# Kernel tuning notes

Measured on AMD Instinct MI355X. Metric: run time of the kernel, lower is better.

The kernel has to match this reference:

```python
import jax, jax.numpy as jnp
import numpy as np

EPS = 1e-8

def setup_inputs() -> dict:
    key = jax.random.key(0)
    k1, k2 = jax.random.split(key)
    x1 = jax.random.normal(k1, (16, 4096, 256), dtype=jnp.float32)
    x2 = jax.random.normal(k2, (16, 4096, 256), dtype=jnp.float32)
    return {"x1": x1, "x2": x2}

def _l2_normalize(x):
    # matches F.normalize / torch norm-with-clamp: x / max(||x||, eps)
    n = jnp.linalg.norm(x, axis=-1, keepdims=True)
    return x / jnp.maximum(n, EPS)

def reference(x1, x2):
    # cosine distance: mean over all segment pairs of (1 - cos_sim)
    # mean_{i,j} (1 - x1n_i . x2n_j) == 1 - (mean_i x1n_i) . (mean_j x2n_j)
    # -- algebraically identical to the original per-batch mm + mean,
    # but avoids materializing the O(n_seg^2) similarity matrix.
    n_batch, embedding_dim = x1.shape[0], x1.shape[-1]
    x1 = x1.reshape(n_batch, -1, embedding_dim)
    x2 = x2.reshape(n_batch, -1, embedding_dim)
    x1n = _l2_normalize(x1)  # (B, S, D)
    x2n = _l2_normalize(x2)
    m1 = x1n.mean(axis=1)    # (B, D)
    m2 = x2n.mean(axis=1)    # (B, D)
    return 1.0 - jnp.einsum('bd,bd->b', m1, m2)  # (B,)
```

## Files before the change

kernel.cpp:

```cpp
#include <hip/hip_runtime.h>


constexpr int D = 256;
constexpr int S = 4096;
constexpr int B = 16;
constexpr int BLOCKS_PER_SEQ = 64;
constexpr int WAVES_PER_BLOCK = 4;
constexpr int WAVES_PER_SEQ  = BLOCKS_PER_SEQ * WAVES_PER_BLOCK;
constexpr int PAIRS_PER_WAVE = (S / 2) / WAVES_PER_SEQ;
constexpr int NSEQ  = 2 * B;
constexpr int NBLK1 = NSEQ * BLOCKS_PER_SEQ;
constexpr float EPS2 = 1e-16f;

template <int CTRL>
__device__ __forceinline__ float dpp_add(float x) {
    int xi = __builtin_bit_cast(int, x);
    int yi = __builtin_amdgcn_update_dpp(0, xi, CTRL, 0xf, 0xf, true);
    return x + __builtin_bit_cast(float, yi);
}

__device__ __forceinline__ float half_reduce(float x) {
    x = dpp_add<0xB1>(x);
    x = dpp_add<0x4E>(x);
    x = dpp_add<0x141>(x);
    x = dpp_add<0x140>(x);
    int xi = __builtin_bit_cast(int, x);
    int yi = __builtin_amdgcn_ds_swizzle(xi, 0x401F);
    return x + __builtin_bit_cast(float, yi);
}

template <bool USE_PARTIALS>
__global__ __launch_bounds__(256) void row_norm_sum_kernel(
    const float* __restrict__ x1, const float* __restrict__ x2,
    float* __restrict__ sums )
{
    const int seq  = blockIdx.x / BLOCKS_PER_SEQ;
    const int blk  = blockIdx.x % BLOCKS_PER_SEQ;
    const int w    = threadIdx.x >> 6;
    const int lane = threadIdx.x & 63;
    const int half = lane >> 5;
    const int l    = lane & 31;
    const int wv   = blk * WAVES_PER_BLOCK + w;

    const int batch = seq >> 1;
    const float* __restrict__ src = (seq & 1) ? x2 : x1;
    const float* base = src + (size_t)batch * S * D
                            + (size_t)(2 * wv + half) * D + 4 * l;

    float4 vlo[PAIRS_PER_WAVE], vhi[PAIRS_PER_WAVE];
    #pragma unroll
    for (int p = 0; p < PAIRS_PER_WAVE; ++p) {
        const float* a = base + (size_t)p * (WAVES_PER_SEQ * 2 * D);
        vlo[p] = *(const float4*)a;
        vhi[p] = *(const float4*)(a + 128);
    }

    float4 acc_lo = make_float4(0.f, 0.f, 0.f, 0.f);
    float4 acc_hi = make_float4(0.f, 0.f, 0.f, 0.f);
    #pragma unroll
    for (int p = 0; p < PAIRS_PER_WAVE; ++p) {
        float ss = vlo[p].x * vlo[p].x + vlo[p].y * vlo[p].y
                 + vlo[p].z * vlo[p].z + vlo[p].w * vlo[p].w
                 + vhi[p].x * vhi[p].x + vhi[p].y * vhi[p].y
                 + vhi[p].z * vhi[p].z + vhi[p].w * vhi[p].w;
        ss = half_reduce(ss);
        const float s = rsqrtf(fmaxf(ss, EPS2));
        acc_lo.x += vlo[p].x * s;  acc_lo.y += vlo[p].y * s;
        acc_lo.z += vlo[p].z * s;  acc_lo.w += vlo[p].w * s;
        acc_hi.x += vhi[p].x * s;  acc_hi.y += vhi[p].y * s;
        acc_hi.z += vhi[p].z * s;  acc_hi.w += vhi[p].w * s;
    }

    __shared__ float red[WAVES_PER_BLOCK][2][D];
    *(float4*)&red[w][half][4 * l]       = acc_lo;
    *(float4*)&red[w][half][128 + 4 * l] = acc_hi;
    __syncthreads();

    const int t = threadIdx.x;
    float val = 0.f;
    #pragma unroll
    for (int ww = 0; ww < WAVES_PER_BLOCK; ++ww)
        val += red[ww][0][t] + red[ww][1][t];
    if (USE_PARTIALS) {
        sums[(size_t)blockIdx.x * D + t] = val;
    } else {
        atomicAdd(&sums[(size_t)seq * D + t], val);
    }
}

__global__ __launch_bounds__(256) void finalize_partials_kernel(
    const float* __restrict__ partials, float* __restrict__ out)
{
    const int b = blockIdx.x;
    const int t = threadIdx.x;
    const int w = t >> 6, lane = t & 63;

    const float* p1 = partials + ((size_t)(2 * b + 0) * BLOCKS_PER_SEQ) * D + t;
    const float* p2 = partials + ((size_t)(2 * b + 1) * BLOCKS_PER_SEQ) * D + t;
    float s1 = 0.f, s2 = 0.f;
    #pragma unroll 8
    for (int k = 0; k < BLOCKS_PER_SEQ; ++k) {
        s1 += p1[(size_t)k * D];
        s2 += p2[(size_t)k * D];
    }
    float d = s1 * s2;
    #pragma unroll
    for (int m = 1; m < 64; m <<= 1) d += __shfl_xor(d, m, 64);

    __shared__ float r[WAVES_PER_BLOCK];
    if (lane == 0) r[w] = d;
    __syncthreads();
    if (t == 0) {
        const float inv = 1.0f / ((float)S * (float)S);
        out[b] = 1.0f - (r[0] + r[1] + r[2] + r[3]) * inv;
    }
}

__global__ __launch_bounds__(64) void finalize_kernel(
    const float* __restrict__ sums, float* __restrict__ out)
{
    const int b = blockIdx.x;
    const int lane = threadIdx.x;
    const float4 a = *(const float4*)(sums + (size_t)(2 * b + 0) * D + lane * 4);
    const float4 c = *(const float4*)(sums + (size_t)(2 * b + 1) * D + lane * 4);
    float d = a.x * c.x + a.y * c.y + a.z * c.z + a.w * c.w;
    #pragma unroll
    for (int m = 1; m < 64; m <<= 1) d += __shfl_xor(d, m, 64);
    if (lane == 0) {
        const float inv = 1.0f / ((float)S * (float)S);
        out[b] = 1.0f - d * inv;
    }
}

extern "C" void kernel_launch(void* const* d_in, const int* in_sizes, int n_in,
                              void* d_out, int out_size, void* d_ws, size_t ws_size,
                              hipStream_t stream) {
    const float* x1 = (const float*)d_in[0];
    const float* x2 = (const float*)d_in[1];
    float* out = (float*)d_out;
    float* ws = (float*)d_ws;

    const size_t partial_bytes = (size_t)NBLK1 * D * sizeof(float);
    if (ws_size >= partial_bytes) {
        row_norm_sum_kernel<true><<<NBLK1, 256, 0, stream>>>(x1, x2, ws);
        finalize_partials_kernel<<<B, 256, 0, stream>>>(ws, out);
    } else {
        hipMemsetAsync(ws, 0, (size_t)NSEQ * D * sizeof(float), stream);
        row_norm_sum_kernel<false><<<NBLK1, 256, 0, stream>>>(x1, x2, ws);
        finalize_kernel<<<B, 64, 0, stream>>>(ws, out);
    }
}
```

Measured before the change: 147.8 us.

## Stream rows through an LDS ring with async global-to-LDS loads

The row-norm kernel now runs one wave per block (2048 blocks of 64 threads), each handling 64 contiguous rows. Rows are loaded with global_load_lds into a four-slot LDS ring, two slots ahead, with explicit vmcnt waits. Before, each wave held 16 rows in registers, all loaded up front. The cross-wave LDS reduction and barrier are replaced by a single cross-half shuffle. The aim is to overlap loads with compute and cut register pressure, at the cost of far fewer resident waves and fewer bytes in flight per CU.

```diff
diff --git a/kernel.cpp b/kernel.cpp
--- a/kernel.cpp
+++ b/kernel.cpp
@@ -4,13 +4,23 @@
 constexpr int D = 256;
 constexpr int S = 4096;
 constexpr int B = 16;
-constexpr int BLOCKS_PER_SEQ = 64;
-constexpr int WAVES_PER_BLOCK = 4;
-constexpr int WAVES_PER_SEQ  = BLOCKS_PER_SEQ * WAVES_PER_BLOCK;
-constexpr int PAIRS_PER_WAVE = (S / 2) / WAVES_PER_SEQ;
-constexpr int NSEQ  = 2 * B;
-constexpr int NBLK1 = NSEQ * BLOCKS_PER_SEQ;
+constexpr int NSEQ = 2 * B;
+constexpr int NROWS = NSEQ * S;
+
+constexpr int NBLK = 2048;
+constexpr int BLOCKS_PER_SEQ = NBLK / NSEQ;
+constexpr int ROWS_PER_BLOCK = NROWS / NBLK;
+constexpr int ROWS_PER_SLOT = 4;
+constexpr int SLOT_BYTES = ROWS_PER_SLOT * D * 4;
+constexpr int NSLOTS = 4;
+constexpr int NITER = ROWS_PER_BLOCK / ROWS_PER_SLOT;
 constexpr float EPS2 = 1e-16f;
+
+__device__ __forceinline__ void dma_row(const float* g, char* lds) {
+    __builtin_amdgcn_global_load_lds(
+        (const __attribute__((address_space(1))) void*)g,
+        (__attribute__((address_space(3))) void*)lds, 16, 0, 0);
+}
 
 template <int CTRL>
 __device__ __forceinline__ float dpp_add(float x) {
@@ -30,61 +40,90 @@
 }
 
 template <bool USE_PARTIALS>
-__global__ __launch_bounds__(256) void row_norm_sum_kernel(
+__global__ __launch_bounds__(64) void row_norm_sum_kernel(
     const float* __restrict__ x1, const float* __restrict__ x2,
     float* __restrict__ sums )
 {
-    const int seq  = blockIdx.x / BLOCKS_PER_SEQ;
-    const int blk  = blockIdx.x % BLOCKS_PER_SEQ;
-    const int w    = threadIdx.x >> 6;
-    const int lane = threadIdx.x & 63;
+    __shared__ char ring[NSLOTS * SLOT_BYTES];
+
+    const int lane = threadIdx.x;
     const int half = lane >> 5;
     const int l    = lane & 31;
-    const int wv   = blk * WAVES_PER_BLOCK + w;
 
-    const int batch = seq >> 1;
-    const float* __restrict__ src = (seq & 1) ? x2 : x1;
-    const float* base = src + (size_t)batch * S * D
-                            + (size_t)(2 * wv + half) * D + 4 * l;
+    const int seq = blockIdx.x / BLOCKS_PER_SEQ;
+    const int r0  = (blockIdx.x % BLOCKS_PER_SEQ) * ROWS_PER_BLOCK;
+    const float* __restrict__ src =
+        ((seq & 1) ? x2 : x1) + (size_t)(seq >> 1) * S * D + (size_t)r0 * D;
+    const float* gl = src + 4 * lane;
 
-    float4 vlo[PAIRS_PER_WAVE], vhi[PAIRS_PER_WAVE];
     #pragma unroll
-    for (int p = 0; p < PAIRS_PER_WAVE; ++p) {
-        const float* a = base + (size_t)p * (WAVES_PER_SEQ * 2 * D);
-        vlo[p] = *(const float4*)a;
-        vhi[p] = *(const float4*)(a + 128);
-    }
+    for (int s = 0; s < 2; ++s)
+        #pragma unroll
+        for (int r = 0; r < ROWS_PER_SLOT; ++r)
+            dma_row(gl + (size_t)(s * ROWS_PER_SLOT + r) * D,
+                    ring + s * SLOT_BYTES + r * 1024);
 
     float4 acc_lo = make_float4(0.f, 0.f, 0.f, 0.f);
     float4 acc_hi = make_float4(0.f, 0.f, 0.f, 0.f);
+
     #pragma unroll
-    for (int p = 0; p < PAIRS_PER_WAVE; ++p) {
-        float ss = vlo[p].x * vlo[p].x + vlo[p].y * vlo[p].y
-                 + vlo[p].z * vlo[p].z + vlo[p].w * vlo[p].w
-                 + vhi[p].x * vhi[p].x + vhi[p].y * vhi[p].y
-                 + vhi[p].z * vhi[p].z + vhi[p].w * vhi[p].w;
-        ss = half_reduce(ss);
-        const float s = rsqrtf(fmaxf(ss, EPS2));
-        acc_lo.x += vlo[p].x * s;  acc_lo.y += vlo[p].y * s;
-        acc_lo.z += vlo[p].z * s;  acc_lo.w += vlo[p].w * s;
-        acc_hi.x += vhi[p].x * s;  acc_hi.y += vhi[p].y * s;
-        acc_hi.z += vhi[p].z * s;  acc_hi.w += vhi[p].w * s;
+    for (int i = 0; i < NITER; ++i) {
+        if (i < NITER - 1) asm volatile("s_waitcnt vmcnt(4)" ::: "memory");
+        else               asm volatile("s_waitcnt vmcnt(0)" ::: "memory");
+
+        if (i + 2 < NITER) {
+            char* sl = ring + ((i + 2) & (NSLOTS - 1)) * SLOT_BYTES;
+            #pragma unroll
+            for (int r = 0; r < ROWS_PER_SLOT; ++r)
+                dma_row(gl + (size_t)((i + 2) * ROWS_PER_SLOT + r) * D,
+                        sl + r * 1024);
+        }
+
+        const char* sl = ring + (i & (NSLOTS - 1)) * SLOT_BYTES;
+        #pragma unroll
+        for (int p = 0; p < 2; ++p) {
+            const float* rowp = (const float*)(sl + p * 2048 + half * 1024);
+            const float4 vlo = *(const float4*)(rowp + 4 * l);
+            const float4 vhi = *(const float4*)(rowp + 128 + 4 * l);
+            float ss = vlo.x * vlo.x + vlo.y * vlo.y
+                     + vlo.z * vlo.z + vlo.w * vlo.w
+                     + vhi.x * vhi.x + vhi.y * vhi.y
+                     + vhi.z * vhi.z + vhi.w * vhi.w;
+            ss = half_reduce(ss);
+            const float sc = rsqrtf(fmaxf(ss, EPS2));
+            acc_lo.x += vlo.x * sc;  acc_lo.y += vlo.y * sc;
+            acc_lo.z += vlo.z * sc;  acc_lo.w += vlo.w * sc;
+            acc_hi.x += vhi.x * sc;  acc_hi.y += vhi.y * sc;
+            acc_hi.z += vhi.z * sc;  acc_hi.w += vhi.w * sc;
+        }
     }
 
-    __shared__ float red[WAVES_PER_BLOCK][2][D];
-    *(float4*)&red[w][half][4 * l]       = acc_lo;
-    *(float4*)&red[w][half][128 + 4 * l] = acc_hi;
-    __syncthreads();
+    float4 tot_lo, tot_hi;
+    tot_lo.x = acc_lo.x + __shfl_xor(acc_lo.x, 32, 64);
+    tot_lo.y = acc_lo.y + __shfl_xor(acc_lo.y, 32, 64);
+    tot_lo.z = acc_lo.z + __shfl_xor(acc_lo.z, 32, 64);
+    tot_lo.w = acc_lo.w + __shfl_xor(acc_lo.w, 32, 64);
+    tot_hi.x = acc_hi.x + __shfl_xor(acc_hi.x, 32, 64);
+    tot_hi.y = acc_hi.y + __shfl_xor(acc_hi.y, 32, 64);
+    tot_hi.z = acc_hi.z + __shfl_xor(acc_hi.z, 32, 64);
+    tot_hi.w = acc_hi.w + __shfl_xor(acc_hi.w, 32, 64);
 
-    const int t = threadIdx.x;
-    float val = 0.f;
-    #pragma unroll
-    for (int ww = 0; ww < WAVES_PER_BLOCK; ++ww)
-        val += red[ww][0][t] + red[ww][1][t];
-    if (USE_PARTIALS) {
-        sums[(size_t)blockIdx.x * D + t] = val;
-    } else {
-        atomicAdd(&sums[(size_t)seq * D + t], val);
+    if (half == 0) {
+        if (USE_PARTIALS) {
+            float* dst = sums + (size_t)blockIdx.x * D;
+            *(float4*)(dst + 4 * l)       = tot_lo;
+            *(float4*)(dst + 128 + 4 * l) = tot_hi;
+        } else {
+            float* dst = sums + (size_t)seq * D;
+            atomicAdd(dst + 4 * l + 0, tot_lo.x);
+            atomicAdd(dst + 4 * l + 1, tot_lo.y);
+            atomicAdd(dst + 4 * l + 2, tot_lo.z);
+            atomicAdd(dst + 4 * l + 3, tot_lo.w);
+            atomicAdd(dst + 128 + 4 * l + 0, tot_hi.x);
+            atomicAdd(dst + 128 + 4 * l + 1, tot_hi.y);
+            atomicAdd(dst + 128 + 4 * l + 2, tot_hi.z);
+            atomicAdd(dst + 128 + 4 * l + 3, tot_hi.w);
+        }
     }
 }
 
@@ -107,7 +146,7 @@
     #pragma unroll
     for (int m = 1; m < 64; m <<= 1) d += __shfl_xor(d, m, 64);
 
-    __shared__ float r[WAVES_PER_BLOCK];
+    __shared__ float r[4];
     if (lane == 0) r[w] = d;
     __syncthreads();
     if (t == 0) {
@@ -140,13 +179,13 @@
     float* out = (float*)d_out;
     float* ws = (float*)d_ws;
 
-    const size_t partial_bytes = (size_t)NBLK1 * D * sizeof(float);
+    const size_t partial_bytes = (size_t)NBLK * D * sizeof(float);
     if (ws_size >= partial_bytes) {
-        row_norm_sum_kernel<true><<<NBLK1, 256, 0, stream>>>(x1, x2, ws);
+        row_norm_sum_kernel<true><<<NBLK, 64, 0, stream>>>(x1, x2, ws);
         finalize_partials_kernel<<<B, 256, 0, stream>>>(ws, out);
     } else {
         hipMemsetAsync(ws, 0, (size_t)NSEQ * D * sizeof(float), stream);
-        row_norm_sum_kernel<false><<<NBLK1, 256, 0, stream>>>(x1, x2, ws);
+        row_norm_sum_kernel<false><<<NBLK, 64, 0, stream>>>(x1, x2, ws);
         finalize_kernel<<<B, 64, 0, stream>>>(ws, out);
     }
 }
```

After: 150.9 us. +2.1%, slower.
